# Kernel optimization log

Hardware: AMD Instinct MI355X
Metric: run time of the kernel (lower is better)

The kernel has to match this reference:

```python
import jax, jax.numpy as jnp
import numpy as np

B, D_IN, D, C = 64, 1024, 768, 1000
EPS = 0.1        # args.alpha_cap
NUM_SIM = 3      # args.num_sim


def setup_inputs() -> dict:
    key = jax.random.key(0)
    k0, k1, k2, k3 = jax.random.split(key, 4)
    return {
        "x": jax.random.normal(k0, (B, D_IN), jnp.float32),
        "W_emb": jax.random.normal(k1, (D, D_IN), jnp.float32) * 0.02,
        "b_emb": jnp.zeros((D,), jnp.float32),
        "W_fc": jax.random.normal(k2, (C, D), jnp.float32) * 0.02,
        "b_fc": jnp.zeros((C,), jnp.float32),
        "anchors": jax.random.normal(k3, (C, D), jnp.float32),
    }


def _forward_core(x, W_emb, b_emb, W_fc, b_fc, anchors):
    # self.embedding(x): feature extractor -> [B, D]
    emb = x @ W_emb.T + b_emb
    # self.model(x) head logits -> [B, C]
    logits = emb @ W_fc.T + b_fc
    # compute_ulb_grads: grad of CE(fc(emb), onehot_j) wrt emb = (softmax - onehot_j) @ W_fc.
    # softmax is shared across all pseudo-labels j, so grad_ij = G_i - W_fc[j].
    p = jax.nn.softmax(logits, axis=-1)          # [B, C]
    G = p @ W_fc                                  # [B, D]
    grads = G[:, None, :] - W_fc[None, :, :]      # [B, C, D]
    # calculate_optimum_alpha: z = anchor - ulb_embed
    z = anchors[None, :, :] - emb[:, None, :]     # [B, C, D]
    z_norm = jnp.linalg.norm(z, axis=-1, keepdims=True)        # [B, C, 1]
    g_norm = jnp.linalg.norm(grads, axis=-1, keepdims=True)    # [B, C, 1]
    alpha = (EPS * z_norm / g_norm) * grads / (z + 1e-8)       # [B, C, D]
    # mix_feature: (1-alpha)*ulb_embed + alpha*anchor
    mix = (1.0 - alpha) * emb[:, None, :] + alpha * anchors[None, :, :]  # [B, C, D]
    # fc(feature_mix) -> [B, C, C]
    logits_mix = jnp.einsum('bjd,cd->bjc', mix, W_fc) + b_fc
    return logits, logits_mix


def reference(x, W_emb, b_emb, W_fc, b_fc, anchors):
    logits, logits_mix = _forward_core(x, W_emb, b_emb, W_fc, b_fc, anchors)
    predictions = jnp.argmax(logits, axis=-1)       # [B]
    preds_mix = jnp.argmax(logits_mix, axis=-1)     # [B, C]
    counts = jnp.zeros((B, C), jnp.float32)
    counts = counts.at[jnp.arange(B), predictions].add(1.0)
    counts = counts.at[jnp.arange(B)[:, None], preds_mix].add(1.0)
    # all_below_threshold: labels_count < num_sample everywhere
    return jnp.all(counts < NUM_SIM, axis=1)
```

## Files before the change

kernel.cpp:

```cpp
#include <hip/hip_runtime.h>
#include <stdint.h>
#include <stddef.h>

#define BB 64
#define DIN 1024
#define DD 768
#define CC 1000
#define EPSA 0.1f
#define NSIM 3

typedef short  s16x8 __attribute__((ext_vector_type(8)));
typedef float  f32x4 __attribute__((ext_vector_type(4)));

static __device__ __forceinline__ unsigned short f2bf_rne(float x) {
  unsigned u = __float_as_uint(x);
  return (unsigned short)((u + 0x7FFFu + ((u >> 16) & 1u)) >> 16);
}
static __device__ __forceinline__ float bf2f(unsigned short h) {
  return __uint_as_float(((unsigned)h) << 16);
}

__global__ __launch_bounds__(256) void prep_kernel(const float* __restrict__ W_fc,
                                                   const float* __restrict__ anchors,
                                                   const float* __restrict__ W_emb,
                                                   const float* __restrict__ x,
                                                   short* __restrict__ Bp, short* __restrict__ Ap,
                                                   short* __restrict__ Ip, short* __restrict__ Xp,
                                                   float* __restrict__ An2) {
  const int blk = blockIdx.x, tid = threadIdx.x;
  if (blk < 1184) {
    const float* src; short* dst; int KS, nrow, gid;
    if (blk < 384)       { src = W_fc;    dst = Bp; KS = 24; nrow = CC;  gid = blk * 256 + tid; }
    else if (blk < 768)  { src = anchors; dst = Ap; KS = 24; nrow = CC;  gid = (blk - 384) * 256 + tid; }
    else if (blk < 1152) { src = W_emb;   dst = Ip; KS = 32; nrow = DD;  gid = (blk - 768) * 256 + tid; }
    else                 { src = x;       dst = Xp; KS = 32; nrow = BB;  gid = (blk - 1152) * 256 + tid; }
    int lane = gid & 63;
    int ks   = (gid >> 6) % KS;
    int nt   = gid / (64 * KS);
    int row  = nt * 16 + (lane & 15);
    int k0   = ks * 32 + (lane >> 4) * 8;
    int stride = KS * 32;
    s16x8 v;
    #pragma unroll
    for (int r = 0; r < 8; ++r) {
      float w = (row < nrow) ? src[(size_t)row * stride + k0 + r] : 0.0f;
      v[r] = (short)f2bf_rne(w);
    }
    ((s16x8*)dst)[gid] = v;
  } else {
    int w = tid >> 6, lane = tid & 63;
    int j = (blk - 1184) * 4 + w;
    const float4* ar = (const float4*)(anchors + (size_t)j * DD);
    float an = 0.f;
    for (int k4 = lane; k4 < DD / 4; k4 += 64) {
      float4 a = ar[k4];
      an += a.x*a.x + a.y*a.y + a.z*a.z + a.w*a.w;
    }
    #pragma unroll
    for (int o = 1; o < 64; o <<= 1) an += __shfl_xor(an, o);
    if (lane == 0) An2[j] = an;
  }
}

__global__ __launch_bounds__(256) void embV_kernel(const short* __restrict__ Bp,
                                                   const short* __restrict__ Ip,
                                                   const short* __restrict__ Xp,
                                                   const float* __restrict__ b_emb,
                                                   unsigned short* __restrict__ Vb,
                                                   short* __restrict__ Vp,
                                                   float* __restrict__ emb,
                                                   short* __restrict__ Ep) {
  const int tid = threadIdx.x, w = tid >> 6, lane = tid & 63;
  __shared__ __attribute__((aligned(16))) short lsh[4608];
  if (blockIdx.x < 256) {
    const int bx = blockIdx.x & 15, cb = blockIdx.x >> 4;
    const int rnt = bx * 4 + w;
    const s16x8* BH = (const s16x8*)Bp;
    f32x4 acc[4] = {};
    for (int ks = 0; ks < 24; ++ks) {
      s16x8 a = BH[(rnt * 24 + ks) * 64 + lane];
      #pragma unroll
      for (int nf = 0; nf < 4; ++nf)
        acc[nf] = __builtin_amdgcn_mfma_f32_16x16x32_bf16(a, BH[((cb * 4 + nf) * 24 + ks) * 64 + lane], acc[nf], 0, 0, 0);
    }
    const int rl0 = (lane >> 4) * 4;
    const int r0 = rnt * 16 + rl0;
    const int c0 = cb * 64 + (lane & 15);
    #pragma unroll
    for (int nf = 0; nf < 4; ++nf)
      #pragma unroll
      for (int rr = 0; rr < 4; ++rr) {
        unsigned short h = f2bf_rne(acc[nf][rr]);
        Vb[(size_t)(r0 + rr) * 1024 + c0 + nf * 16] = h;
        lsh[w * 1152 + (rl0 + rr) * 72 + (lane & 15) + nf * 16] = (short)h;
      }
    __syncthreads();
    #pragma unroll
    for (int ksh = 0; ksh < 2; ++ksh) {
      int ks = cb * 2 + ksh;
      s16x8 v = *(const s16x8*)&lsh[w * 1152 + (lane & 15) * 72 + ksh * 32 + (lane >> 4) * 8];
      ((s16x8*)Vp)[(rnt * 32 + ks) * 64 + lane] = v;
    }
  } else {
    const int g = blockIdx.x - 256;
    const int nfr = g * 4 + w;
    const s16x8* XH = (const s16x8*)Xp;
    const s16x8* IH = (const s16x8*)Ip;
    f32x4 acc[4] = {};
    for (int ks = 0; ks < 32; ++ks) {
      s16x8 b = IH[(nfr * 32 + ks) * 64 + lane];
      #pragma unroll
      for (int mt = 0; mt < 4; ++mt)
        acc[mt] = __builtin_amdgcn_mfma_f32_16x16x32_bf16(XH[(mt * 32 + ks) * 64 + lane], b, acc[mt], 0, 0, 0);
    }
    const int d = nfr * 16 + (lane & 15);
    const int dl = w * 16 + (lane & 15);
    const float be = b_emb[d];
    #pragma unroll
    for (int mt = 0; mt < 4; ++mt)
      #pragma unroll
      for (int rr = 0; rr < 4; ++rr) {
        int b = mt * 16 + (lane >> 4) * 4 + rr;
        float ev = acc[mt][rr] + be;
        emb[(size_t)b * DD + d] = ev;
        lsh[b * 72 + dl] = (short)f2bf_rne(ev);
      }
    __syncthreads();
    #pragma unroll
    for (int ksh = 0; ksh < 2; ++ksh) {
      int ks = g * 2 + ksh;
      int mt2 = tid >> 6;
      s16x8 v = *(const s16x8*)&lsh[(mt2 * 16 + (lane & 15)) * 72 + ksh * 32 + (lane >> 4) * 8];
      ((s16x8*)Ep)[(mt2 * 24 + ks) * 64 + lane] = v;
    }
  }
}

__global__ __launch_bounds__(64) void logitsAE_kernel(const short* __restrict__ Ep,
                                                      const short* __restrict__ Bp,
                                                      const short* __restrict__ Ap,
                                                      const float* __restrict__ b_fc,
                                                      float* __restrict__ logits,
                                                      float* __restrict__ AE) {
  const int nfr = blockIdx.x;
  const int mt  = blockIdx.y;
  const int lane = threadIdx.x;
  const s16x8* E = (const s16x8*)Ep;
  const s16x8* B = (const s16x8*)Bp;
  const s16x8* A = (const s16x8*)Ap;
  f32x4 accL = {}, accA = {};
  for (int ks = 0; ks < 24; ++ks) {
    s16x8 a  = E[(mt * 24 + ks) * 64 + lane];
    s16x8 bW = B[(nfr * 24 + ks) * 64 + lane];
    s16x8 bA = A[(nfr * 24 + ks) * 64 + lane];
    accL = __builtin_amdgcn_mfma_f32_16x16x32_bf16(a, bW, accL, 0, 0, 0);
    accA = __builtin_amdgcn_mfma_f32_16x16x32_bf16(a, bA, accA, 0, 0, 0);
  }
  const int c = nfr * 16 + (lane & 15);
  if (c < CC) {
    const float bf = b_fc[c];
    #pragma unroll
    for (int rr = 0; rr < 4; ++rr) {
      int b = mt * 16 + (lane >> 4) * 4 + rr;
      logits[b * CC + c] = accL[rr] + bf;
      AE[b * CC + c]     = accA[rr];
    }
  }
}

__global__ __launch_bounds__(256) void softmax_kernel(const float* __restrict__ logits,
                                                      const float* __restrict__ emb,
                                                      float* __restrict__ p,
                                                      short* __restrict__ Pp,
                                                      int* __restrict__ pred,
                                                      float* __restrict__ En2) {
  int b = blockIdx.x, t = threadIdx.x;
  __shared__ float smax[256];
  __shared__ int   sidx[256];
  __shared__ float ssum[256];
  {
    float pe = 0.f;
    for (int k = t; k < DD; k += 256) { float e = emb[b * DD + k]; pe += e * e; }
    #pragma unroll
    for (int o = 1; o < 64; o <<= 1) pe += __shfl_xor(pe, o);
    __shared__ float se[4];
    if ((t & 63) == 0) se[t >> 6] = pe;
    __syncthreads();
    if (t == 0) En2[b] = se[0] + se[1] + se[2] + se[3];
  }
  float m = -3.402823466e38f; int mi = 0;
  for (int c = t; c < CC; c += 256) {
    float v = logits[b * CC + c];
    if (v > m) { m = v; mi = c; }
  }
  smax[t] = m; sidx[t] = mi;
  __syncthreads();
  for (int o = 128; o > 0; o >>= 1) {
    if (t < o) {
      float v2 = smax[t + o]; int i2 = sidx[t + o];
      if (v2 > smax[t] || (v2 == smax[t] && i2 < sidx[t])) { smax[t] = v2; sidx[t] = i2; }
    }
    __syncthreads();
  }
  float M = smax[0];
  if (t == 0) pred[b] = sidx[0];
  float sum = 0.f;
  for (int c = t; c < CC; c += 256) sum += expf(logits[b * CC + c] - M);
  ssum[t] = sum;
  __syncthreads();
  for (int o = 128; o > 0; o >>= 1) {
    if (t < o) ssum[t] += ssum[t + o];
    __syncthreads();
  }
  float S = ssum[0];
  const int mt = b >> 4, blo = b & 15;
  for (int j = t; j < CC; j += 256) {
    float pj = expf(logits[b * CC + j] - M) / S;
    p[b * CC + j] = pj;
    size_t fi = ((size_t)(mt * 32 + (j >> 5)) * 64 + ((j >> 3) & 3) * 16 + blo) * 8 + (j & 7);
    Pp[fi] = (short)f2bf_rne(pj);
  }
  if (t < 24) {
    int j = 1000 + t;
    size_t fi = ((size_t)(mt * 32 + (j >> 5)) * 64 + ((j >> 3) & 3) * 16 + blo) * 8 + (j & 7);
    Pp[fi] = 0;
  }
}

__global__ __launch_bounds__(64) void u_kernel(const short* __restrict__ Pp,
                                               const short* __restrict__ Vp,
                                               float* __restrict__ u) {
  const int nfr = blockIdx.x;
  const int mt  = blockIdx.y;
  const int lane = threadIdx.x;
  const s16x8* P = (const s16x8*)Pp;
  const s16x8* V = (const s16x8*)Vp;
  f32x4 acc = {};
  for (int ks = 0; ks < 32; ++ks) {
    s16x8 b = V[(nfr * 32 + ks) * 64 + lane];
    acc = __builtin_amdgcn_mfma_f32_16x16x32_bf16(P[(mt * 32 + ks) * 64 + lane], b, acc, 0, 0, 0);
  }
  const int c = nfr * 16 + (lane & 15);
  if (c < CC) {
    #pragma unroll
    for (int rr = 0; rr < 4; ++rr)
      u[(mt * 16 + (lane >> 4) * 4 + rr) * CC + c] = acc[rr];
  }
}

__global__ __launch_bounds__(256) void scan_kernel(const float* __restrict__ logits,
                                                   const float* __restrict__ u,
                                                   const float* __restrict__ p,
                                                   const float* __restrict__ AE,
                                                   const float* __restrict__ An2,
                                                   const float* __restrict__ En2,
                                                   const unsigned short* __restrict__ Vb,
                                                   unsigned long long* __restrict__ part) {
  const int b = blockIdx.x, cz = blockIdx.y;
  const int tid = threadIdx.x;
  const int c0 = cz * 63;
  const int cend = (CC - c0 < 63) ? (CC - c0) : 63;
  __shared__ __attribute__((aligned(8))) float2 LU[64];
  __shared__ float se[4];

  if (tid < cend) {
    int c = c0 + tid;
    LU[tid] = float2{logits[b * CC + c], u[b * CC + c]};
  }
  float partsum = 0.f;
  {
    int cg = tid * 4;
    if (cg + 3 < CC) {
      float4 p4 = *(const float4*)(p + b * CC + cg);
      float4 u4 = *(const float4*)(u + b * CC + cg);
      partsum = p4.x*u4.x + p4.y*u4.y + p4.z*u4.z + p4.w*u4.w;
    } else {
      #pragma unroll
      for (int i = 0; i < 4; ++i) {
        int c = cg + i;
        if (c < CC) partsum += p[b * CC + c] * u[b * CC + c];
      }
    }
  }
  #pragma unroll
  for (int o = 1; o < 64; o <<= 1) partsum += __shfl_xor(partsum, o);
  if ((tid & 63) == 0) se[tid >> 6] = partsum;
  __syncthreads();
  const float gn2b = se[0] + se[1] + se[2] + se[3];
  const float en2 = En2[b];

  const int jt = (tid < 250 ? tid : 249) * 4;
  float4 an4 = *(const float4*)(An2 + jt);
  float4 ae4 = *(const float4*)(AE + b * CC + jt);
  float4 uj4 = *(const float4*)(u + b * CC + jt);
  float sj[4], nsj[4];
  {
    float anv[4] = {an4.x, an4.y, an4.z, an4.w};
    float aev[4] = {ae4.x, ae4.y, ae4.z, ae4.w};
    float ujv[4] = {uj4.x, uj4.y, uj4.z, uj4.w};
    #pragma unroll
    for (int k = 0; k < 4; ++k) {
      float vd  = bf2f(Vb[(size_t)(jt + k) * 1024 + jt + k]);
      float zn2 = anv[k] - 2.0f * aev[k] + en2;
      float gn2 = gn2b - 2.0f * ujv[k] + vd;
      sj[k] = (EPSA * sqrtf(zn2)) / sqrtf(gn2);
      nsj[k] = -sj[k];
    }
  }

  float best[4] = {-3.402823466e38f, -3.402823466e38f, -3.402823466e38f, -3.402823466e38f};
  int   bi[4]   = {0, 0, 0, 0};
  const unsigned short* Vcol = Vb + jt;
  #pragma unroll 7
  for (int i = 0; i < cend; ++i) {
    int c = c0 + i;
    float2 lu = LU[i];
    uint2 vv = *(const uint2*)(Vcol + (size_t)c * 1024);
    float v0 = __uint_as_float(vv.x << 16);
    float v1 = __uint_as_float(vv.x & 0xffff0000u);
    float v2 = __uint_as_float(vv.y << 16);
    float v3 = __uint_as_float(vv.y & 0xffff0000u);
    float t0 = fmaf(sj[0], lu.y, lu.x);
    float t1 = fmaf(sj[1], lu.y, lu.x);
    float t2 = fmaf(sj[2], lu.y, lu.x);
    float t3 = fmaf(sj[3], lu.y, lu.x);
    float val0 = fmaf(nsj[0], v0, t0);
    float val1 = fmaf(nsj[1], v1, t1);
    float val2 = fmaf(nsj[2], v2, t2);
    float val3 = fmaf(nsj[3], v3, t3);
    if (val0 > best[0]) { best[0] = val0; bi[0] = c; }
    if (val1 > best[1]) { best[1] = val1; bi[1] = c; }
    if (val2 > best[2]) { best[2] = val2; bi[2] = c; }
    if (val3 > best[3]) { best[3] = val3; bi[3] = c; }
  }

  if (tid < 250) {
    unsigned long long* dst = part + (size_t)cz * 64000 + b * 1000 + jt;
    #pragma unroll
    for (int k = 0; k < 4; ++k) {
      unsigned ub = __float_as_uint(best[k]);
      ub = (ub & 0x80000000u) ? ~ub : (ub | 0x80000000u);
      dst[k] = ((unsigned long long)ub << 32) |
               (unsigned long long)(0xFFFFFFFFu - (unsigned)bi[k]);
    }
  }
}

__global__ __launch_bounds__(256) void counts_kernel(const unsigned long long* __restrict__ part,
                                                     const int* __restrict__ pred,
                                                     float* __restrict__ out) {
  int b = blockIdx.x, t = threadIdx.x;
  __shared__ int cnt[CC];
  __shared__ int bad;
  for (int c = t; c < CC; c += 256) cnt[c] = 0;
  if (t == 0) bad = 0;
  __syncthreads();
  if (t == 0) atomicAdd(&cnt[pred[b]], 1);
  const unsigned long long* pr = part + b * 1000;
  for (int j = t; j < CC; j += 256) {
    unsigned long long key = 0;
    #pragma unroll
    for (int cz = 0; cz < 16; ++cz) {
      unsigned long long k2 = pr[(size_t)cz * 64000 + j];
      key = (k2 > key) ? k2 : key;
    }
    int c = (int)(0xFFFFFFFFu - (unsigned)(key & 0xFFFFFFFFull));
    atomicAdd(&cnt[c], 1);
  }
  __syncthreads();
  for (int c = t; c < CC; c += 256) if (cnt[c] >= NSIM) bad = 1;
  __syncthreads();
  if (t == 0) out[b] = bad ? 0.0f : 1.0f;
}

extern "C" void kernel_launch(void* const* d_in, const int* in_sizes, int n_in,
                              void* d_out, int out_size, void* d_ws, size_t ws_size,
                              hipStream_t stream) {
  const float* x       = (const float*)d_in[0];
  const float* W_emb   = (const float*)d_in[1];
  const float* b_emb   = (const float*)d_in[2];
  const float* W_fc    = (const float*)d_in[3];
  const float* b_fc    = (const float*)d_in[4];
  const float* anchors = (const float*)d_in[5];
  float* out = (float*)d_out;

  float* emb    = (float*)d_ws;
  float* logits = emb + BB * DD;
  float* p      = logits + BB * CC;
  float* u      = p + BB * CC;
  float* AE     = u + BB * CC;
  float* An2    = AE + BB * CC;
  float* En2    = An2 + 1024;
  int*   pred   = (int*)(En2 + 64);
  unsigned long long* part = (unsigned long long*)(pred + 64);
  short* Bp     = (short*)(part + 16 * 64000);
  short* Ap     = Bp + 64 * 24 * 64 * 8;
  short* Ip     = Ap + 64 * 24 * 64 * 8;
  short* Xp     = Ip + 48 * 32 * 64 * 8;
  short* Ep     = Xp + 4 * 32 * 64 * 8;
  short* Pp     = Ep + 4 * 24 * 64 * 8;
  unsigned short* Vb = (unsigned short*)(Pp + 4 * 32 * 64 * 8);
  short* Vp     = (short*)(Vb + 1024 * 1024);

  hipLaunchKernelGGL(prep_kernel,    dim3(1434), dim3(256), 0, stream,
                     W_fc, anchors, W_emb, x, Bp, Ap, Ip, Xp, An2);
  hipLaunchKernelGGL(embV_kernel,    dim3(268), dim3(256), 0, stream,
                     Bp, Ip, Xp, b_emb, Vb, Vp, emb, Ep);
  hipLaunchKernelGGL(logitsAE_kernel,dim3(64, 4), dim3(64), 0, stream, Ep, Bp, Ap, b_fc, logits, AE);
  hipLaunchKernelGGL(softmax_kernel, dim3(BB), dim3(256), 0, stream, logits, emb, p, Pp, pred, En2);
  hipLaunchKernelGGL(u_kernel,       dim3(64, 4), dim3(64), 0, stream, Pp, Vp, u);
  hipLaunchKernelGGL(scan_kernel,    dim3(BB, 16), dim3(256), 0, stream,
                     logits, u, p, AE, An2, En2, Vb, part);
  hipLaunchKernelGGL(counts_kernel,  dim3(BB), dim3(256), 0, stream, part, pred, out);
}
```

Before: 73.37 us.

## Use wave-shuffle reductions in softmax and transpose partial-argmax buffer layout

The softmax kernel now reduces max/argmax and the embedding norm with wave shuffles instead of shared-memory tree loops, keeps logits in registers and caches exp values in shared memory so expf runs once per element. The partial argmax buffer is transposed so each (b,j) holds its 16 chunk results contiguously, making the counts kernel read one contiguous run per row. The scan kernel's writes become strided by 16, which may hurt store coalescing there.

```diff
diff --git a/kernel.cpp b/kernel.cpp
--- a/kernel.cpp
+++ b/kernel.cpp
@@ -174,48 +174,57 @@
                                                       short* __restrict__ Pp,
                                                       int* __restrict__ pred,
                                                       float* __restrict__ En2) {
-  int b = blockIdx.x, t = threadIdx.x;
-  __shared__ float smax[256];
-  __shared__ int   sidx[256];
-  __shared__ float ssum[256];
-  {
-    float pe = 0.f;
-    for (int k = t; k < DD; k += 256) { float e = emb[b * DD + k]; pe += e * e; }
-    #pragma unroll
-    for (int o = 1; o < 64; o <<= 1) pe += __shfl_xor(pe, o);
-    __shared__ float se[4];
-    if ((t & 63) == 0) se[t >> 6] = pe;
-    __syncthreads();
-    if (t == 0) En2[b] = se[0] + se[1] + se[2] + se[3];
-  }
+  const int b = blockIdx.x, t = threadIdx.x;
+  const int w = t >> 6, lane = t & 63;
+  __shared__ float ex[CC];
+  __shared__ float sm[4]; __shared__ int si[4]; __shared__ float ss[4];
+  __shared__ float sM, sS;
+
+  float pe = 0.f;
+  for (int k = t; k < DD; k += 256) { float e = emb[b * DD + k]; pe += e * e; }
   float m = -3.402823466e38f; int mi = 0;
-  for (int c = t; c < CC; c += 256) {
-    float v = logits[b * CC + c];
+  float lv[4];
+  #pragma unroll
+  for (int i = 0; i < 4; ++i) {
+    int c = t + i * 256;
+    float v = (c < CC) ? logits[b * CC + c] : -3.402823466e38f;
+    lv[i] = v;
     if (v > m) { m = v; mi = c; }
   }
-  smax[t] = m; sidx[t] = mi;
-  __syncthreads();
-  for (int o = 128; o > 0; o >>= 1) {
-    if (t < o) {
-      float v2 = smax[t + o]; int i2 = sidx[t + o];
-      if (v2 > smax[t] || (v2 == smax[t] && i2 < sidx[t])) { smax[t] = v2; sidx[t] = i2; }
-    }
-    __syncthreads();
-  }
-  float M = smax[0];
-  if (t == 0) pred[b] = sidx[0];
+  #pragma unroll
+  for (int o = 1; o < 64; o <<= 1) {
+    float ov = __shfl_xor(m, o); int oi = __shfl_xor(mi, o);
+    if (ov > m || (ov == m && oi < mi)) { m = ov; mi = oi; }
+    pe += __shfl_xor(pe, o);
+  }
+  if (lane == 0) { sm[w] = m; si[w] = mi; ss[w] = pe; }
+  __syncthreads();
+  if (t == 0) {
+    float M = sm[0]; int Mi = si[0];
+    #pragma unroll
+    for (int ww = 1; ww < 4; ++ww)
+      if (sm[ww] > M || (sm[ww] == M && si[ww] < Mi)) { M = sm[ww]; Mi = si[ww]; }
+    sM = M; pred[b] = Mi;
+    En2[b] = ss[0] + ss[1] + ss[2] + ss[3];
+  }
+  __syncthreads();
+  const float M = sM;
   float sum = 0.f;
-  for (int c = t; c < CC; c += 256) sum += expf(logits[b * CC + c] - M);
-  ssum[t] = sum;
-  __syncthreads();
-  for (int o = 128; o > 0; o >>= 1) {
-    if (t < o) ssum[t] += ssum[t + o];
-    __syncthreads();
-  }
-  float S = ssum[0];
+  #pragma unroll
+  for (int i = 0; i < 4; ++i) {
+    int c = t + i * 256;
+    if (c < CC) { float e = expf(lv[i] - M); ex[c] = e; sum += e; }
+  }
+  #pragma unroll
+  for (int o = 1; o < 64; o <<= 1) sum += __shfl_xor(sum, o);
+  if (lane == 0) ss[w] = sum;
+  __syncthreads();
+  if (t == 0) sS = ss[0] + ss[1] + ss[2] + ss[3];
+  __syncthreads();
+  const float S = sS;
   const int mt = b >> 4, blo = b & 15;
   for (int j = t; j < CC; j += 256) {
-    float pj = expf(logits[b * CC + j] - M) / S;
+    float pj = ex[j] / S;
     p[b * CC + j] = pj;
     size_t fi = ((size_t)(mt * 32 + (j >> 5)) * 64 + ((j >> 3) & 3) * 16 + blo) * 8 + (j & 7);
     Pp[fi] = (short)f2bf_rne(pj);
@@ -335,13 +344,13 @@
   }
 
   if (tid < 250) {
-    unsigned long long* dst = part + (size_t)cz * 64000 + b * 1000 + jt;
+    unsigned long long* dst = part + ((size_t)(b * 1000 + jt)) * 16 + cz;
     #pragma unroll
     for (int k = 0; k < 4; ++k) {
       unsigned ub = __float_as_uint(best[k]);
       ub = (ub & 0x80000000u) ? ~ub : (ub | 0x80000000u);
-      dst[k] = ((unsigned long long)ub << 32) |
-               (unsigned long long)(0xFFFFFFFFu - (unsigned)bi[k]);
+      dst[(size_t)k * 16] = ((unsigned long long)ub << 32) |
+                            (unsigned long long)(0xFFFFFFFFu - (unsigned)bi[k]);
     }
   }
 }
@@ -356,12 +365,12 @@
   if (t == 0) bad = 0;
   __syncthreads();
   if (t == 0) atomicAdd(&cnt[pred[b]], 1);
-  const unsigned long long* pr = part + b * 1000;
   for (int j = t; j < CC; j += 256) {
-    unsigned long long key = 0;
-    #pragma unroll
-    for (int cz = 0; cz < 16; ++cz) {
-      unsigned long long k2 = pr[(size_t)cz * 64000 + j];
+    const unsigned long long* q = part + ((size_t)(b * 1000 + j)) * 16;
+    unsigned long long key = q[0];
+    #pragma unroll
+    for (int cz = 1; cz < 16; ++cz) {
+      unsigned long long k2 = q[cz];
       key = (k2 > key) ? k2 : key;
     }
     int c = (int)(0xFFFFFFFFu - (unsigned)(key & 0xFFFFFFFFull));
@@ -393,7 +402,7 @@
   float* En2    = An2 + 1024;
   int*   pred   = (int*)(En2 + 64);
   unsigned long long* part = (unsigned long long*)(pred + 64);
-  short* Bp     = (short*)(part + 16 * 64000);
+  short* Bp     = (short*)(part + 64000 * 16);
   short* Ap     = Bp + 64 * 24 * 64 * 8;
   short* Ip     = Ap + 64 * 24 * 64 * 8;
   short* Xp     = Ip + 48 * 32 * 64 * 8;
```

After: 74.37 us. About the same (+1.4%).
